# Kernel optimization log

Hardware: AMD Instinct MI355X
Metric: run time of the kernel (lower is better)

## Reference

```python
import jax, jax.numpy as jnp
import numpy as np

B, T, E, H = 2, 2048, 1024, 4
Dk = E // H          # 256 head qk dim
Dv = Dk * 2          # 512 head v dim (expansion_ratio=2)
EPS = 1e-5
ROPE_BASE = 10000.0


def setup_inputs() -> dict:
    key = jax.random.key(0)
    ks = jax.random.split(key, 7)
    s = 0.02  # small init matching xavier gains in reset_parameters
    return {
        "x": jax.random.normal(ks[0], (B, T, E), jnp.float32),
        "Wq": jax.random.normal(ks[1], (E, E), jnp.float32) * s,
        "Wk": jax.random.normal(ks[2], (E, E), jnp.float32) * s,
        "Wv": jax.random.normal(ks[3], (E, 2 * E), jnp.float32) * s,
        "Wg": jax.random.normal(ks[4], (E, 2 * E), jnp.float32) * s,
        "Wo": jax.random.normal(ks[5], (2 * E, E), jnp.float32) * s,
        "gn_weight": jnp.ones((Dv,), jnp.float32),
    }


def _rotary(q, k):
    # q,k: [b, t, h, d]; non-interleaved (GPT-NeoX) rotary over the full head dim
    d = q.shape[-1]
    inv_freq = 1.0 / (ROPE_BASE ** (jnp.arange(0, d, 2, dtype=jnp.float32) / d))
    t = jnp.arange(q.shape[1], dtype=jnp.float32)
    freqs = jnp.einsum('t,f->tf', t, inv_freq)      # [t, d/2]
    cos = jnp.cos(freqs)[None, :, None, :]
    sin = jnp.sin(freqs)[None, :, None, :]

    def rot(x):
        x1, x2 = x[..., : d // 2], x[..., d // 2:]
        return jnp.concatenate([x1 * cos - x2 * sin, x2 * cos + x1 * sin], axis=-1)

    return rot(q), rot(k)


def reference(x, Wq, Wk, Wv, Wg, Wo, gn_weight):
    b, t, e = x.shape
    q = (x @ Wq).reshape(b, t, H, Dk)
    k = (x @ Wk).reshape(b, t, H, Dk)
    q, k = _rotary(q, k)
    q = q.transpose(0, 2, 1, 3) * (Dk ** -0.5)      # [b,h,t,dk], scale = head_qk_dim^-0.5
    k = k.transpose(0, 2, 1, 3)
    v = (x @ Wv).reshape(b, t, H, Dv).transpose(0, 2, 1, 3)  # [b,h,t,dv]

    # RetNet per-head decay: gamma_h = 1 - 2^-(5+h)
    gamma = 1.0 - jnp.exp2(-5.0 - jnp.arange(H, dtype=jnp.float32))
    ti = jnp.arange(t)
    n = ti[:, None] - ti[None, :]                   # t - s
    decay = jnp.where(
        n >= 0,
        gamma[:, None, None] ** jnp.maximum(n, 0).astype(jnp.float32),
        0.0,
    )                                               # [h,t,t] causal decayed mask

    scores = jnp.einsum('bhtd,bhsd->bhts', q, k) * decay[None]
    o = jnp.einsum('bhts,bhsd->bhtd', scores, v)    # [b,h,t,dv]
    o = o.transpose(0, 2, 1, 3)                     # [b,t,h,dv]

    # per-head RMSNorm (group_norm over head_v_dim)
    rms = jnp.sqrt(jnp.mean(o * o, axis=-1, keepdims=True) + EPS)
    o = o / rms * gn_weight

    # NOTE: the given source multiplies by raw g_proj(x) (gate_fn not applied in forward)
    g = x @ Wg                                      # [b,t,2E]
    return (o.reshape(b, t, H * Dv) * g) @ Wo       # [b,t,E]
```

## Files before the change

kernel.cpp:

```cpp
#include <hip/hip_runtime.h>
#include <hip/hip_bf16.h>

#define B_ 2
#define T_ 2048
#define E_ 1024
#define DK 256
#define DV 512
#define MROWS 4096
#define LDQKVG 6144
#define CHK 128
#define NCHK 16

typedef __attribute__((ext_vector_type(8))) short short8;
typedef __attribute__((ext_vector_type(4))) short short4v;
typedef __attribute__((ext_vector_type(4))) float floatx4;

typedef __attribute__((address_space(3))) unsigned as3_u32;
typedef const __attribute__((address_space(1))) unsigned as1_u32;

static __device__ __forceinline__ void gld_lds16(const unsigned short* gsrc, unsigned short* ldst) {
  __builtin_amdgcn_global_load_lds((as1_u32*)gsrc, (as3_u32*)ldst, 16, 0, 0);
}

static __device__ __forceinline__ float bf2f(unsigned short u) {
  union { unsigned int i; float f; } x; x.i = ((unsigned int)u) << 16; return x.f;
}
static __device__ __forceinline__ unsigned short f2bf(float f) {
  __hip_bfloat16 h = __float2bfloat16(f);
  return __builtin_bit_cast(unsigned short, h);
}

__global__ void __launch_bounds__(256) prep_kernel(
    const float* __restrict__ x, unsigned short* __restrict__ xb,
    const float* __restrict__ Wq, const float* __restrict__ Wk,
    const float* __restrict__ Wv, const float* __restrict__ Wg,
    unsigned short* __restrict__ WallT,
    const float* __restrict__ Wo, unsigned short* __restrict__ WoT,
    float2* __restrict__ ropetab) {
  __shared__ float tile[32][33];
  int bid = blockIdx.x;
  int tid = threadIdx.x;
  if (bid < 2048) {
    int i = bid * 256 + tid;
    size_t base = (size_t)i * 8;
    float4 a = *(const float4*)(x + base);
    float4 b = *(const float4*)(x + base + 4);
    short8 o;
    o[0] = (short)f2bf(a.x); o[1] = (short)f2bf(a.y);
    o[2] = (short)f2bf(a.z); o[3] = (short)f2bf(a.w);
    o[4] = (short)f2bf(b.x); o[5] = (short)f2bf(b.y);
    o[6] = (short)f2bf(b.z); o[7] = (short)f2bf(b.w);
    *(short8*)(xb + base) = o;
    return;
  }
  if (bid < 8192) {
    bid -= 2048;
    const float* in; unsigned short* o; int ldin, nbx;
    if (bid < 1024)      { in = Wq; o = WallT;                       ldin = 1024; nbx = 32; }
    else if (bid < 2048) { in = Wk; o = WallT + (size_t)1024 * 1024; ldin = 1024; nbx = 32; bid -= 1024; }
    else if (bid < 4096) { in = Wv; o = WallT + (size_t)2048 * 1024; ldin = 2048; nbx = 64; bid -= 2048; }
    else                 { in = Wg; o = WallT + (size_t)4096 * 1024; ldin = 2048; nbx = 64; bid -= 4096; }
    int c0 = (bid % nbx) * 32, r0 = (bid / nbx) * 32;
    int tx = tid & 31, ty = tid >> 5;
#pragma unroll
    for (int i = 0; i < 32; i += 8)
      tile[ty + i][tx] = in[(size_t)(r0 + ty + i) * ldin + c0 + tx];
    __syncthreads();
#pragma unroll
    for (int i = 0; i < 32; i += 8)
      o[(size_t)(c0 + ty + i) * 1024 + r0 + tx] = f2bf(tile[tx][ty + i]);
    return;
  }
  if (bid < 9216) {
    int idx = (bid - 8192) * 256 + tid;
    int t = idx >> 7, j = idx & 127;
    float invf = exp2f(-(float)j * (13.287712379549449f / 128.0f));
    float ang = (float)t * invf;
    ropetab[idx] = make_float2(cosf(ang), sinf(ang));
    return;
  }
  {
    int lb = bid - 9216;
    int c0 = (lb & 31) * 32, r0 = (lb >> 5) * 32;
    int tx = tid & 31, ty = tid >> 5;
#pragma unroll
    for (int i = 0; i < 32; i += 8)
      tile[ty + i][tx] = Wo[(size_t)(r0 + ty + i) * 1024 + c0 + tx];
    __syncthreads();
#pragma unroll
    for (int i = 0; i < 32; i += 8)
      WoT[(size_t)(c0 + ty + i) * 2048 + r0 + tx] = f2bf(tile[tx][ty + i]);
  }
}

template<int BM, int BN, int WM_W, int WN_W, int MINW, bool F32OUT>
__global__ void __launch_bounds__(WM_W * WN_W * 64, MINW) gemmp_kernel(
    const unsigned short* __restrict__ A, int lda,
    const unsigned short* __restrict__ Bt, int ldb, int K,
    void* __restrict__ Cp, int ldc, int ccol0, int nbx) {
  constexpr int WAVES = WM_W * WN_W;
  constexpr int AG = BM / 16 / WAVES;
  constexpr int BG = BN / 16 / WAVES;
  constexpr int RM = BM / WM_W;
  constexpr int CN = BN / WN_W;
  constexpr int MB = RM / 16, NB = CN / 16;
  __shared__ __align__(16) unsigned short lds[3][(BM + BN) * 32];
  const int tid = threadIdx.x;
  const int lane = tid & 63;
  const int wid = tid >> 6;
  const int wm = wid / WN_W, wn = wid % WN_W;
  const int bid = blockIdx.x;
  const int m0 = (bid % nbx) * BM;
  const int n0 = (bid / nbx) * BN;
  const unsigned short* Ab = A + (size_t)m0 * lda;
  const unsigned short* Bb = Bt + (size_t)n0 * ldb;
  const int NT = K / 32;

  auto stage = [&](int sl, int t) {
    const int k0 = t * 32;
#pragma unroll
    for (int j = 0; j < AG; ++j) {
      int g = wid * AG + j;
      int ci = g * 64 + lane;
      int row = ci >> 2, c = ci & 3;
      int cs = c ^ ((row >> 1) & 3);
      gld_lds16(Ab + (size_t)row * lda + k0 + cs * 8, &lds[sl][g * 512]);
    }
#pragma unroll
    for (int j = 0; j < BG; ++j) {
      int g = wid * BG + j;
      int ci = g * 64 + lane;
      int row = ci >> 2, c = ci & 3;
      int cs = c ^ ((row >> 1) & 3);
      gld_lds16(Bb + (size_t)row * ldb + k0 + cs * 8, &lds[sl][BM * 32 + g * 512]);
    }
  };

  floatx4 acc[MB][NB];
#pragma unroll
  for (int i = 0; i < MB; i++)
#pragma unroll
    for (int j = 0; j < NB; j++)
      acc[i][j] = (floatx4){0.f, 0.f, 0.f, 0.f};

  stage(0, 0);
  stage(1, 1);

  int cur = 0;
#pragma unroll 1
  for (int t = 0; t < NT; ++t) {
    if (t + 1 < NT) {
      if constexpr (AG + BG == 2) asm volatile("s_waitcnt vmcnt(2)" ::: "memory");
      else if constexpr (AG + BG == 3) asm volatile("s_waitcnt vmcnt(3)" ::: "memory");
      else if constexpr (AG + BG == 4) asm volatile("s_waitcnt vmcnt(4)" ::: "memory");
      else if constexpr (AG + BG == 6) asm volatile("s_waitcnt vmcnt(6)" ::: "memory");
      else asm volatile("s_waitcnt vmcnt(8)" ::: "memory");
    } else {
      asm volatile("s_waitcnt vmcnt(0)" ::: "memory");
    }
    __builtin_amdgcn_s_barrier();
    asm volatile("" ::: "memory");
    int sl = cur + 2; if (sl >= 3) sl -= 3;
    if (t + 2 < NT) stage(sl, t + 2);

    const unsigned short* As_ = lds[cur];
    const unsigned short* Bs_ = lds[cur] + BM * 32;
    short8 af[MB], bfv[NB];
#pragma unroll
    for (int i = 0; i < MB; ++i) {
      int row = wm * RM + i * 16 + (lane & 15);
      af[i] = *(const short8*)&As_[row * 32 + (((lane >> 4) ^ ((row >> 1) & 3)) * 8)];
    }
#pragma unroll
    for (int j = 0; j < NB; ++j) {
      int nn = wn * CN + j * 16 + (lane & 15);
      bfv[j] = *(const short8*)&Bs_[nn * 32 + (((lane >> 4) ^ ((nn >> 1) & 3)) * 8)];
    }
#pragma unroll
    for (int i = 0; i < MB; ++i)
#pragma unroll
      for (int j = 0; j < NB; ++j)
        acc[i][j] = __builtin_amdgcn_mfma_f32_16x16x32_bf16(af[i], bfv[j], acc[i][j], 0, 0, 0);
    cur = cur + 1 == 3 ? 0 : cur + 1;
  }

#pragma unroll
  for (int i = 0; i < MB; ++i)
#pragma unroll
    for (int j = 0; j < NB; ++j)
#pragma unroll
      for (int r = 0; r < 4; ++r) {
        int row = m0 + wm * RM + i * 16 + (lane >> 4) * 4 + r;
        int col = ccol0 + n0 + wn * CN + j * 16 + (lane & 15);
        float v = acc[i][j][r];
        if (F32OUT) ((float*)Cp)[(size_t)row * ldc + col] = v;
        else ((unsigned short*)Cp)[(size_t)row * ldc + col] = f2bf(v);
      }
}

__global__ void __launch_bounds__(256) postproc_kernel(
    unsigned short* __restrict__ qkvg, const float2* __restrict__ tab,
    unsigned short* __restrict__ kTs, unsigned short* __restrict__ vT) {
  __shared__ unsigned short kt[256][33];
  __shared__ unsigned short vt[512][33];
  const int tid = threadIdx.x;
  const int rt = blockIdx.x >> 2, h = blockIdx.x & 3;
  const int grow0 = rt * 32;
  const float lg = log2f(1.0f - exp2f(-5.0f - (float)h));
  const int r = tid >> 3;
  const int grow = grow0 + r;
  const int t = grow & (T_ - 1);
  const float sq = 0.0625f * exp2f((float)(t & (CHK - 1)) * lg);
  const float fac = exp2f((float)(CHK - (t & (CHK - 1))) * lg);
#pragma unroll
  for (int half = 0; half < 2; ++half) {
    int j0 = (tid & 7) * 8 + half * 64;
    size_t base = (size_t)grow * LDQKVG + h * DK + j0;
    short8 q1 = *(const short8*)&qkvg[base],      q2 = *(const short8*)&qkvg[base + 128];
    short8 k1 = *(const short8*)&qkvg[base + E_], k2 = *(const short8*)&qkvg[base + E_ + 128];
    short8 oq1, oq2, ok1, ok2;
#pragma unroll
    for (int e = 0; e < 8; ++e) {
      float2 cs = tab[(t << 7) + j0 + e];
      float c = cs.x, s = cs.y;
      float a1 = bf2f((unsigned short)q1[e]), a2 = bf2f((unsigned short)q2[e]);
      float b1 = bf2f((unsigned short)k1[e]), b2 = bf2f((unsigned short)k2[e]);
      float rk1 = b1 * c - b2 * s, rk2 = b2 * c + b1 * s;
      oq1[e] = (short)f2bf((a1 * c - a2 * s) * sq);
      oq2[e] = (short)f2bf((a2 * c + a1 * s) * sq);
      ok1[e] = (short)f2bf(rk1);
      ok2[e] = (short)f2bf(rk2);
      kt[j0 + e][r]       = f2bf(rk1 * fac);
      kt[j0 + e + 128][r] = f2bf(rk2 * fac);
    }
    *(short8*)&qkvg[base]            = oq1;
    *(short8*)&qkvg[base + 128]      = oq2;
    *(short8*)&qkvg[base + E_]       = ok1;
    *(short8*)&qkvg[base + E_ + 128] = ok2;
  }
  __syncthreads();
  {
    int dk = tid;
    unsigned short* dst = kTs + (size_t)(h * DK + dk) * MROWS + grow0;
#pragma unroll
    for (int i = 0; i < 4; ++i) {
      short8 w;
#pragma unroll
      for (int e = 0; e < 8; ++e) w[e] = (short)kt[dk][i * 8 + e];
      *(short8*)(dst + i * 8) = w;
    }
  }
  {
    int cv = tid & 7;
#pragma unroll
    for (int i = 0; i < 8; ++i) {
      int col = cv * 64 + i * 8;
      short8 v = *(const short8*)&qkvg[(size_t)grow * LDQKVG + 2048 + h * DV + col];
#pragma unroll
      for (int e = 0; e < 8; ++e) vt[col + e][r] = (unsigned short)v[e];
    }
  }
  __syncthreads();
#pragma unroll
  for (int p = 0; p < 2; ++p) {
    int dv = p * 256 + tid;
    unsigned short* dst = vT + (size_t)(h * DV + dv) * MROWS + grow0;
#pragma unroll
    for (int i = 0; i < 4; ++i) {
      short8 w;
#pragma unroll
      for (int e = 0; e < 8; ++e) w[e] = (short)vt[dv][i * 8 + e];
      *(short8*)(dst + i * 8) = w;
    }
  }
}

__global__ void __launch_bounds__(256) state_kernel(
    const unsigned short* __restrict__ kTs, const unsigned short* __restrict__ vT,
    unsigned short* __restrict__ Sbuf) {
  const int lane = threadIdx.x & 63, wid = threadIdx.x >> 6;
  const int bh = blockIdx.x & 7, dkt = (blockIdx.x >> 3) & 3, dvt = (blockIdx.x >> 5) & 15;
  const int b = bh >> 2, h = bh & 3;
  const float lg = log2f(1.0f - exp2f(-5.0f - (float)h));
  const float g128 = exp2f((float)CHK * lg);
  const int dk0 = dkt * 64 + wid * 16;
  const int dv0 = dvt * 32;
  const unsigned short* arow = kTs + (size_t)(h * DK + dk0 + (lane & 15)) * MROWS + b * T_ + (lane >> 4) * 8;
  const unsigned short* brow = vT + (size_t)(h * DV + dv0 + (lane & 15)) * MROWS + b * T_ + (lane >> 4) * 8;
  floatx4 acc[2];
  acc[0] = (floatx4){0.f, 0.f, 0.f, 0.f};
  acc[1] = (floatx4){0.f, 0.f, 0.f, 0.f};
#pragma unroll 4
  for (int c = 0; c < NCHK; ++c) {
    size_t sb = (size_t)(c * 8 + bh) * (DV * DK);
#pragma unroll
    for (int nb = 0; nb < 2; ++nb) {
      short4v o;
#pragma unroll
      for (int r = 0; r < 4; ++r) o[r] = (short)f2bf(acc[nb][r]);
      *(short4v*)&Sbuf[sb + (size_t)(dv0 + nb * 16 + (lane & 15)) * DK + dk0 + (lane >> 4) * 4] = o;
    }
#pragma unroll
    for (int nb = 0; nb < 2; ++nb)
#pragma unroll
      for (int r = 0; r < 4; ++r) acc[nb][r] *= g128;
#pragma unroll
    for (int ks = 0; ks < 4; ++ks) {
      short8 a = *(const short8*)(arow + c * CHK + ks * 32);
#pragma unroll
      for (int nb = 0; nb < 2; ++nb) {
        short8 bb = *(const short8*)(brow + (size_t)nb * 16 * MROWS + c * CHK + ks * 32);
        acc[nb] = __builtin_amdgcn_mfma_f32_16x16x32_bf16(a, bb, acc[nb], 0, 0, 0);
      }
    }
  }
}

__global__ void __launch_bounds__(256, 3) retention2_kernel(
    const unsigned short* __restrict__ qkvg, const unsigned short* __restrict__ vT,
    const unsigned short* __restrict__ Sbuf, const float* __restrict__ gnw,
    unsigned short* __restrict__ og, float* __restrict__ ssbuf) {
  __shared__ unsigned short k_lds[32 * 256];
  __shared__ unsigned short v_lds[256 * 32];
  __shared__ unsigned short s_lds[4][16 * 40];
  const int tid = threadIdx.x, lane = tid & 63, wid = tid >> 6;
  const int bh  = blockIdx.x & 7;
  const int c   = (blockIdx.x >> 3) & 15;
  const int dvh = (blockIdx.x >> 7) & 1;
  const int rhf = (blockIdx.x >> 8) & 1;
  const int b = bh >> 2, h = bh & 3;
  const float lg = log2f(1.0f - exp2f(-5.0f - (float)h));
  const int rb0 = b * T_ + c * CHK + rhf * 64;
  const int taub = rhf * 64 + wid * 16;
  const int nst = rhf ? 4 : 2;
  const unsigned short* kbase = qkvg + (size_t)(b * T_ + c * CHK) * LDQKVG + E_ + h * DK;
  const unsigned short* vbase = vT + (size_t)(h * DV + dvh * 256) * MROWS + b * T_ + c * CHK;
  const unsigned short* Sp = Sbuf + (size_t)(c * 8 + bh) * (DV * DK) + (size_t)dvh * 256 * DK;

  auto stage = [&](int st) {
    int s0 = st * 32;
#pragma unroll
    for (int j = 0; j < 4; ++j) {
      int ci = (wid * 4 + j) * 64 + lane;
      int row = ci >> 5, cc = ci & 31;
      int cs = cc ^ (row & 7);
      gld_lds16(kbase + (size_t)(s0 + row) * LDQKVG + cs * 8, &k_lds[(wid * 4 + j) * 512]);
    }
#pragma unroll
    for (int j = 0; j < 4; ++j) {
      int ci = (wid * 4 + j) * 64 + lane;
      int dv = ci >> 2, cc = ci & 3;
      int cs = cc ^ ((dv ^ (dv >> 2)) & 3);
      gld_lds16(vbase + (size_t)dv * MROWS + s0 + cs * 8, &v_lds[(wid * 4 + j) * 512]);
    }
  };

  stage(0);

  short8 qf[8];
  {
    int qrow = rb0 + wid * 16 + (lane & 15);
    const unsigned short* qp = qkvg + (size_t)qrow * LDQKVG + h * DK + (lane >> 4) * 8;
#pragma unroll
    for (int kk = 0; kk < 8; kk++) qf[kk] = *(const short8*)(qp + kk * 32);
  }
  floatx4 oacc[16];
#pragma unroll
  for (int nb = 0; nb < 16; ++nb) oacc[nb] = (floatx4){0.f, 0.f, 0.f, 0.f};
#pragma unroll
  for (int ks = 0; ks < 8; ++ks) {
#pragma unroll
    for (int nb = 0; nb < 16; ++nb) {
      short8 sf = *(const short8*)&Sp[(size_t)(nb * 16 + (lane & 15)) * DK + ks * 32 + (lane >> 4) * 8];
      oacc[nb] = __builtin_amdgcn_mfma_f32_16x16x32_bf16(qf[ks], sf, oacc[nb], 0, 0, 0);
    }
  }

#pragma unroll 1
  for (int st = 0; st < nst; ++st) {
    __syncthreads();
#pragma unroll
    for (int ch = 0; ch < 2; ++ch) {
      floatx4 f = (floatx4){0.f, 0.f, 0.f, 0.f};
      const int srow = ch * 16 + (lane & 15);
      __builtin_amdgcn_s_setprio(1);
#pragma unroll
      for (int kk = 0; kk < 8; kk++) {
        int cc = (kk * 4 + (lane >> 4)) ^ (srow & 7);
        short8 kf = *(const short8*)&k_lds[srow * 256 + cc * 8];
        f = __builtin_amdgcn_mfma_f32_16x16x32_bf16(qf[kk], kf, f, 0, 0, 0);
      }
      __builtin_amdgcn_s_setprio(0);
#pragma unroll
      for (int r = 0; r < 4; ++r) {
        int lr = (lane >> 4) * 4 + r;
        int sig = st * 32 + ch * 16 + (lane & 15);
        int n = taub + lr - sig;
        float val = (n >= 0) ? f[r] * exp2f(-(float)sig * lg) : 0.0f;
        s_lds[wid][lr * 40 + ch * 16 + (lane & 15)] = f2bf(val);
      }
    }
    short8 af = *(const short8*)&s_lds[wid][(lane & 15) * 40 + (lane >> 4) * 8];
    __builtin_amdgcn_s_setprio(1);
#pragma unroll
    for (int nb = 0; nb < 16; ++nb) {
      int dv = nb * 16 + (lane & 15);
      int cc = (lane >> 4) ^ ((dv ^ (dv >> 2)) & 3);
      short8 vf = *(const short8*)&v_lds[dv * 32 + cc * 8];
      oacc[nb] = __builtin_amdgcn_mfma_f32_16x16x32_bf16(af, vf, oacc[nb], 0, 0, 0);
    }
    __builtin_amdgcn_s_setprio(0);
    if (st + 1 < nst) {
      __syncthreads();
      stage(st + 1);
    }
  }
#pragma unroll
  for (int r = 0; r < 4; ++r) {
    float ss = 0.f;
#pragma unroll
    for (int nb = 0; nb < 16; nb++) { float xv = oacc[nb][r]; ss += xv * xv; }
    ss += __shfl_xor(ss, 1, 64);
    ss += __shfl_xor(ss, 2, 64);
    ss += __shfl_xor(ss, 4, 64);
    ss += __shfl_xor(ss, 8, 64);
    if ((lane & 15) == 0) {
      int row = rb0 + wid * 16 + (lane >> 4) * 4 + r;
      ssbuf[(size_t)row * 8 + h * 2 + dvh] = ss;
    }
  }
#pragma unroll
  for (int r = 0; r < 4; ++r) {
    int row = rb0 + wid * 16 + (lane >> 4) * 4 + r;
    size_t growbase = (size_t)row * LDQKVG + 4096 + h * DV + dvh * 256;
    size_t orowbase = (size_t)row * LDQKVG + h * DV + dvh * 256;
#pragma unroll
    for (int nb = 0; nb < 16; nb++) {
      int col = nb * 16 + (lane & 15);
      float gv = bf2f(qkvg[growbase + col]);
      og[orowbase + col] = f2bf(oacc[nb][r] * gnw[dvh * 256 + col] * gv);
    }
  }
}

__global__ void __launch_bounds__(256) normalize_kernel(
    unsigned short* __restrict__ og, const float* __restrict__ ssbuf) {
  int i = blockIdx.x * 256 + threadIdx.x;
  size_t e0 = (size_t)i * 8;
  int row = (int)(e0 >> 11);
  int col = (int)(e0 & 2047);
  int h = col >> 9;
  float ss = ssbuf[(size_t)row * 8 + h * 2] + ssbuf[(size_t)row * 8 + h * 2 + 1];
  float inv = rsqrtf(ss * (1.0f / 512.0f) + 1e-5f);
  size_t a = (size_t)row * LDQKVG + col;
  short8 v = *(const short8*)(og + a);
#pragma unroll
  for (int j = 0; j < 8; j++) v[j] = (short)f2bf(bf2f((unsigned short)v[j]) * inv);
  *(short8*)(og + a) = v;
}

extern "C" void kernel_launch(void* const* d_in, const int* in_sizes, int n_in,
                              void* d_out, int out_size, void* d_ws, size_t ws_size,
                              hipStream_t stream) {
  const float* x   = (const float*)d_in[0];
  const float* Wq  = (const float*)d_in[1];
  const float* Wk  = (const float*)d_in[2];
  const float* Wv  = (const float*)d_in[3];
  const float* Wg  = (const float*)d_in[4];
  const float* Wo  = (const float*)d_in[5];
  const float* gnw = (const float*)d_in[6];
  float* out = (float*)d_out;

  char* ws = (char*)d_ws;
  size_t off = 0;
  auto alloc = [&](size_t bytes) { char* p = ws + off; off += (bytes + 255) & ~(size_t)255; return p; };
  unsigned short* qkvg = (unsigned short*)alloc((size_t)MROWS * LDQKVG * 2);
  unsigned short* vT   = (unsigned short*)alloc((size_t)2048 * MROWS * 2);
  char* regS = alloc((size_t)NCHK * 8 * DV * DK * 2);
  unsigned short* Sbuf  = (unsigned short*)regS;
  unsigned short* xb    = (unsigned short*)regS;
  unsigned short* WallT = (unsigned short*)(regS + 8388608);
  unsigned short* kTs = (unsigned short*)alloc((size_t)1024 * MROWS * 2);
  unsigned short* WoT = (unsigned short*)alloc((size_t)1024 * 2048 * 2);
  float2* ropetab = (float2*)alloc((size_t)T_ * 128 * 8);
  float* ssbuf = (float*)alloc((size_t)MROWS * 8 * 4);
  unsigned short* og = qkvg + 2048;

  prep_kernel<<<11264, 256, 0, stream>>>(x, xb, Wq, Wk, Wv, Wg, WallT, Wo, WoT, ropetab);

  gemmp_kernel<128, 128, 2, 2, 3, false><<<1536, 256, 0, stream>>>(
      xb, 1024, WallT, 1024, 1024, qkvg, LDQKVG, 0, 32);

  postproc_kernel<<<512, 256, 0, stream>>>(qkvg, ropetab, kTs, vT);

  state_kernel<<<512, 256, 0, stream>>>(kTs, vT, Sbuf);

  retention2_kernel<<<512, 256, 0, stream>>>(qkvg, vT, Sbuf, gnw, og, ssbuf);

  normalize_kernel<<<4096, 256, 0, stream>>>(og, ssbuf);

  gemmp_kernel<128, 128, 2, 2, 3, true><<<256, 256, 0, stream>>>(
      og, LDQKVG, WoT, 2048, 2048, out, E_, 0, 32);
}
```

Before: 218.9 us.

## Fuse RMS normalization into retention kernel with full-Dv blocks; retile QKVG GEMM

```diff
diff --git a/kernel.cpp b/kernel.cpp
--- a/kernel.cpp
+++ b/kernel.cpp
@@ -316,26 +316,25 @@
   }
 }
 
-__global__ void __launch_bounds__(256, 3) retention2_kernel(
+__global__ void __launch_bounds__(256) retention3_kernel(
     const unsigned short* __restrict__ qkvg, const unsigned short* __restrict__ vT,
     const unsigned short* __restrict__ Sbuf, const float* __restrict__ gnw,
-    unsigned short* __restrict__ og, float* __restrict__ ssbuf) {
+    unsigned short* __restrict__ og) {
   __shared__ unsigned short k_lds[32 * 256];
-  __shared__ unsigned short v_lds[256 * 32];
+  __shared__ unsigned short v_lds[512 * 32];
   __shared__ unsigned short s_lds[4][16 * 40];
   const int tid = threadIdx.x, lane = tid & 63, wid = tid >> 6;
   const int bh  = blockIdx.x & 7;
   const int c   = (blockIdx.x >> 3) & 15;
-  const int dvh = (blockIdx.x >> 7) & 1;
-  const int rhf = (blockIdx.x >> 8) & 1;
+  const int rhf = (blockIdx.x >> 7) & 1;
   const int b = bh >> 2, h = bh & 3;
   const float lg = log2f(1.0f - exp2f(-5.0f - (float)h));
   const int rb0 = b * T_ + c * CHK + rhf * 64;
   const int taub = rhf * 64 + wid * 16;
   const int nst = rhf ? 4 : 2;
   const unsigned short* kbase = qkvg + (size_t)(b * T_ + c * CHK) * LDQKVG + E_ + h * DK;
-  const unsigned short* vbase = vT + (size_t)(h * DV + dvh * 256) * MROWS + b * T_ + c * CHK;
-  const unsigned short* Sp = Sbuf + (size_t)(c * 8 + bh) * (DV * DK) + (size_t)dvh * 256 * DK;
+  const unsigned short* vbase = vT + (size_t)(h * DV) * MROWS + b * T_ + c * CHK;
+  const unsigned short* Sp = Sbuf + (size_t)(c * 8 + bh) * (DV * DK);
 
   auto stage = [&](int st) {
     int s0 = st * 32;
@@ -347,11 +346,11 @@
       gld_lds16(kbase + (size_t)(s0 + row) * LDQKVG + cs * 8, &k_lds[(wid * 4 + j) * 512]);
     }
 #pragma unroll
-    for (int j = 0; j < 4; ++j) {
-      int ci = (wid * 4 + j) * 64 + lane;
+    for (int j = 0; j < 8; ++j) {
+      int ci = (wid * 8 + j) * 64 + lane;
       int dv = ci >> 2, cc = ci & 3;
       int cs = cc ^ ((dv ^ (dv >> 2)) & 3);
-      gld_lds16(vbase + (size_t)dv * MROWS + s0 + cs * 8, &v_lds[(wid * 4 + j) * 512]);
+      gld_lds16(vbase + (size_t)dv * MROWS + s0 + cs * 8, &v_lds[(wid * 8 + j) * 512]);
     }
   };
 
@@ -364,13 +363,13 @@
 #pragma unroll
     for (int kk = 0; kk < 8; kk++) qf[kk] = *(const short8*)(qp + kk * 32);
   }
-  floatx4 oacc[16];
-#pragma unroll
-  for (int nb = 0; nb < 16; ++nb) oacc[nb] = (floatx4){0.f, 0.f, 0.f, 0.f};
+  floatx4 oacc[32];
+#pragma unroll
+  for (int nb = 0; nb < 32; ++nb) oacc[nb] = (floatx4){0.f, 0.f, 0.f, 0.f};
 #pragma unroll
   for (int ks = 0; ks < 8; ++ks) {
 #pragma unroll
-    for (int nb = 0; nb < 16; ++nb) {
+    for (int nb = 0; nb < 32; ++nb) {
       short8 sf = *(const short8*)&Sp[(size_t)(nb * 16 + (lane & 15)) * DK + ks * 32 + (lane >> 4) * 8];
       oacc[nb] = __builtin_amdgcn_mfma_f32_16x16x32_bf16(qf[ks], sf, oacc[nb], 0, 0, 0);
     }
@@ -403,7 +402,7 @@
     short8 af = *(const short8*)&s_lds[wid][(lane & 15) * 40 + (lane >> 4) * 8];
     __builtin_amdgcn_s_setprio(1);
 #pragma unroll
-    for (int nb = 0; nb < 16; ++nb) {
+    for (int nb = 0; nb < 32; ++nb) {
       int dv = nb * 16 + (lane & 15);
       int cc = (lane >> 4) ^ ((dv ^ (dv >> 2)) & 3);
       short8 vf = *(const short8*)&v_lds[dv * 32 + cc * 8];
@@ -419,44 +418,22 @@
   for (int r = 0; r < 4; ++r) {
     float ss = 0.f;
 #pragma unroll
-    for (int nb = 0; nb < 16; nb++) { float xv = oacc[nb][r]; ss += xv * xv; }
+    for (int nb = 0; nb < 32; nb++) { float xv = oacc[nb][r]; ss += xv * xv; }
     ss += __shfl_xor(ss, 1, 64);
     ss += __shfl_xor(ss, 2, 64);
     ss += __shfl_xor(ss, 4, 64);
     ss += __shfl_xor(ss, 8, 64);
-    if ((lane & 15) == 0) {
-      int row = rb0 + wid * 16 + (lane >> 4) * 4 + r;
-      ssbuf[(size_t)row * 8 + h * 2 + dvh] = ss;
-    }
-  }
-#pragma unroll
-  for (int r = 0; r < 4; ++r) {
+    float inv = rsqrtf(ss * (1.0f / 512.0f) + 1e-5f);
     int row = rb0 + wid * 16 + (lane >> 4) * 4 + r;
-    size_t growbase = (size_t)row * LDQKVG + 4096 + h * DV + dvh * 256;
-    size_t orowbase = (size_t)row * LDQKVG + h * DV + dvh * 256;
-#pragma unroll
-    for (int nb = 0; nb < 16; nb++) {
+    size_t growbase = (size_t)row * LDQKVG + 4096 + h * DV;
+    size_t orowbase = (size_t)row * LDQKVG + h * DV;
+#pragma unroll
+    for (int nb = 0; nb < 32; nb++) {
       int col = nb * 16 + (lane & 15);
       float gv = bf2f(qkvg[growbase + col]);
-      og[orowbase + col] = f2bf(oacc[nb][r] * gnw[dvh * 256 + col] * gv);
-    }
-  }
-}
-
-__global__ void __launch_bounds__(256) normalize_kernel(
-    unsigned short* __restrict__ og, const float* __restrict__ ssbuf) {
-  int i = blockIdx.x * 256 + threadIdx.x;
-  size_t e0 = (size_t)i * 8;
-  int row = (int)(e0 >> 11);
-  int col = (int)(e0 & 2047);
-  int h = col >> 9;
-  float ss = ssbuf[(size_t)row * 8 + h * 2] + ssbuf[(size_t)row * 8 + h * 2 + 1];
-  float inv = rsqrtf(ss * (1.0f / 512.0f) + 1e-5f);
-  size_t a = (size_t)row * LDQKVG + col;
-  short8 v = *(const short8*)(og + a);
-#pragma unroll
-  for (int j = 0; j < 8; j++) v[j] = (short)f2bf(bf2f((unsigned short)v[j]) * inv);
-  *(short8*)(og + a) = v;
+      og[orowbase + col] = f2bf(oacc[nb][r] * inv * gnw[col] * gv);
+    }
+  }
 }
 
 extern "C" void kernel_launch(void* const* d_in, const int* in_sizes, int n_in,
@@ -483,21 +460,18 @@
   unsigned short* kTs = (unsigned short*)alloc((size_t)1024 * MROWS * 2);
   unsigned short* WoT = (unsigned short*)alloc((size_t)1024 * 2048 * 2);
   float2* ropetab = (float2*)alloc((size_t)T_ * 128 * 8);
-  float* ssbuf = (float*)alloc((size_t)MROWS * 8 * 4);
   unsigned short* og = qkvg + 2048;
 
   prep_kernel<<<11264, 256, 0, stream>>>(x, xb, Wq, Wk, Wv, Wg, WallT, Wo, WoT, ropetab);
 
-  gemmp_kernel<128, 128, 2, 2, 3, false><<<1536, 256, 0, stream>>>(
+  gemmp_kernel<128, 256, 2, 4, 4, false><<<768, 512, 0, stream>>>(
       xb, 1024, WallT, 1024, 1024, qkvg, LDQKVG, 0, 32);
 
   postproc_kernel<<<512, 256, 0, stream>>>(qkvg, ropetab, kTs, vT);
 
   state_kernel<<<512, 256, 0, stream>>>(kTs, vT, Sbuf);
 
-  retention2_kernel<<<512, 256, 0, stream>>>(qkvg, vT, Sbuf, gnw, og, ssbuf);
-
-  normalize_kernel<<<4096, 256, 0, stream>>>(og, ssbuf);
+  retention3_kernel<<<256, 256, 0, stream>>>(qkvg, vT, Sbuf, gnw, og);
 
   gemmp_kernel<128, 128, 2, 2, 3, true><<<256, 256, 0, stream>>>(
       og, LDQKVG, WoT, 2048, 2048, out, E_, 0, 32);
```

Result: faster. 211.6 us, median of 7 (-3.3%).
